# Optimization experiments

Measured on AMD Instinct MI355X. Metric: run time of the kernel, lower is better.

The kernel has to match this reference:

```python
import jax, jax.numpy as jnp
import numpy as np

B, I, H = 4096, 1024, 1024


def setup_inputs() -> dict:
    key = jax.random.key(0)
    ks = jax.random.split(key, 7)
    s = 0.1  # matches uniform(-0.1, 0.1) init scale loosely
    return {
        "input": jax.random.normal(ks[0], (B, I), jnp.float32),
        "h_t": jax.random.normal(ks[1], (B, H), jnp.float32),
        "c_t": jax.random.normal(ks[2], (B, H), jnp.float32),
        "w_i": jax.random.uniform(ks[3], (I, 4 * H), jnp.float32, -s, s),
        "w_h": jax.random.uniform(ks[4], (H, 4 * H), jnp.float32, -s, s),
        "b_i": jax.random.uniform(ks[5], (4 * H,), jnp.float32, -s, s),
        "b_h": jax.random.uniform(ks[6], (4 * H,), jnp.float32, -s, s),
    }


def reference(input, h_t, c_t, w_i, w_h, b_i, b_h):
    # ifgo: [B, 4H] = x @ w_i + h @ w_h + b_i + b_h
    ifgo = input @ w_i + h_t @ w_h + (b_i + b_h)
    i, f, g, o = jnp.split(ifgo, 4, axis=1)
    i = jax.nn.sigmoid(i)
    f = jax.nn.sigmoid(f)
    g = jnp.tanh(g)
    o = jax.nn.sigmoid(o)
    c_new = f * c_t + i * g
    h_new = o * jnp.tanh(c_new)
    return (h_new, c_new)
```

## Files before the change

### kernel.cpp

```cpp
#include <hip/hip_runtime.h>
#include <stdint.h>

typedef __attribute__((ext_vector_type(8))) short short8;
typedef __attribute__((ext_vector_type(4))) float floatx4;

__device__ inline unsigned short f2bf(float x) {
  union { float f; unsigned int u; } v; v.f = x;
  unsigned int r = v.u + 0x7FFFu + ((v.u >> 16) & 1u);
  return (unsigned short)(r >> 16);
}

__global__ void pack_a(const float* __restrict__ x, const float* __restrict__ h,
                       unsigned short* __restrict__ A) {
  int idx = blockIdx.x * 256 + threadIdx.x;
  int row = idx >> 8;
  int kc  = (idx & 255) << 3;
  const float* src = (kc < 1024) ? (x + (size_t)row * 1024 + kc)
                                 : (h + (size_t)row * 1024 + (kc - 1024));
  float4 a = ((const float4*)src)[0];
  float4 b = ((const float4*)src)[1];
  uint4 o;
  o.x = f2bf(a.x) | ((unsigned)f2bf(a.y) << 16);
  o.y = f2bf(a.z) | ((unsigned)f2bf(a.w) << 16);
  o.z = f2bf(b.x) | ((unsigned)f2bf(b.y) << 16);
  o.w = f2bf(b.z) | ((unsigned)f2bf(b.w) << 16);
  *(uint4*)(A + (size_t)row * 2048 + kc) = o;
}

__global__ void pack_w(const float* __restrict__ wi, const float* __restrict__ wh,
                       unsigned short* __restrict__ Wt) {
  __shared__ float tile[64][65];
  int kt = blockIdx.x & 31;
  int nt = blockIdx.x >> 5;
  int k0 = kt << 6, n0 = nt << 6;
  const float* src = (k0 < 1024) ? (wi + (size_t)k0 * 4096)
                                 : (wh + (size_t)(k0 - 1024) * 4096);
  int t = threadIdx.x;
  int c4 = (t & 15) << 2, rr = t >> 4;
#pragma unroll
  for (int p = 0; p < 4; ++p) {
    int kk = rr + p * 16;
    float4 v = *(const float4*)(src + (size_t)kk * 4096 + n0 + c4);
    tile[kk][c4 + 0] = v.x; tile[kk][c4 + 1] = v.y;
    tile[kk][c4 + 2] = v.z; tile[kk][c4 + 3] = v.w;
  }
  __syncthreads();
  int k8 = (t & 7) << 3, nn = t >> 3;
#pragma unroll
  for (int p = 0; p < 2; ++p) {
    int n = nn + p * 32;
    uint4 o;
    o.x = f2bf(tile[k8 + 0][n]) | ((unsigned)f2bf(tile[k8 + 1][n]) << 16);
    o.y = f2bf(tile[k8 + 2][n]) | ((unsigned)f2bf(tile[k8 + 3][n]) << 16);
    o.z = f2bf(tile[k8 + 4][n]) | ((unsigned)f2bf(tile[k8 + 5][n]) << 16);
    o.w = f2bf(tile[k8 + 6][n]) | ((unsigned)f2bf(tile[k8 + 7][n]) << 16);
    *(uint4*)(Wt + (size_t)(n0 + n) * 2048 + k0 + k8) = o;
  }
}

__device__ inline void gl_lds16(const void* g, void* l) {
  __builtin_amdgcn_global_load_lds(
      (const __attribute__((address_space(1))) void*)g,
      (__attribute__((address_space(3))) void*)l, 16, 0, 0);
}

__global__ void gemm_bt(const unsigned short* __restrict__ A,
                        const unsigned short* __restrict__ Bt,
                        float* __restrict__ C) {
  constexpr int K = 2048, N = 4096;
  __shared__ char AsB[128 * 64];
  __shared__ char BsB[128 * 64];
  const int tid  = threadIdx.x;
  const int lane = tid & 63;
  const int wave = tid >> 6;
  const int wm = wave >> 1, wn = wave & 1;
  const int m0 = blockIdx.y << 7, n0 = blockIdx.x << 7;

  const int r  = tid >> 2;
  const int cb = (tid & 3) << 4;
  const char* aS0 = (const char*)A + (size_t)(m0 + r) * K * 2 + cb;
  const char* aS1 = aS0 + (size_t)64 * K * 2;
  const char* bS0 = (const char*)Bt + (size_t)(n0 + r) * K * 2 + cb;
  const char* bS1 = bS0 + (size_t)64 * K * 2;
  char* aD0 = AsB + tid * 16;
  char* aD1 = AsB + 4096 + tid * 16;
  char* bD0 = BsB + tid * 16;
  char* bD1 = BsB + 4096 + tid * 16;

  floatx4 acc[4][4] = {};
  const int rA = (wm << 6) + (lane & 15);
  const int rB = (wn << 6) + (lane & 15);
  const int kb = (lane >> 4) << 4;

  for (int ks = 0; ks < K; ks += 32) {
    gl_lds16(aS0, aD0); gl_lds16(aS1, aD1);
    gl_lds16(bS0, bD0); gl_lds16(bS1, bD1);
    aS0 += 64; aS1 += 64; bS0 += 64; bS1 += 64;
    __syncthreads();
    short8 af[4], bfr[4];
#pragma unroll
    for (int f = 0; f < 4; ++f) {
      af[f]  = *(const short8*)(AsB + (rA + f * 16) * 64 + kb);
      bfr[f] = *(const short8*)(BsB + (rB + f * 16) * 64 + kb);
    }
#pragma unroll
    for (int i = 0; i < 4; ++i)
#pragma unroll
      for (int j = 0; j < 4; ++j)
        acc[i][j] = __builtin_amdgcn_mfma_f32_16x16x32_bf16(af[i], bfr[j], acc[i][j], 0, 0, 0);
    __syncthreads();
  }

  const int er = (lane >> 4) << 2;
  const int ec = lane & 15;
#pragma unroll
  for (int i = 0; i < 4; ++i) {
#pragma unroll
    for (int rg = 0; rg < 4; ++rg) {
      int row = m0 + (wm << 6) + i * 16 + er + rg;
      float* cp = C + (size_t)row * N + n0 + (wn << 6) + ec;
#pragma unroll
      for (int j = 0; j < 4; ++j) cp[j * 16] = acc[i][j][rg];
    }
  }
}

__device__ inline float sigm(float x)  { return 1.0f / (1.0f + __expf(-x)); }
__device__ inline float tanhx(float x) { return 2.0f / (1.0f + __expf(-2.0f * x)) - 1.0f; }

__global__ void lstm_ew(const float* __restrict__ ifgo, const float* __restrict__ ct,
                        const float* __restrict__ bi, const float* __restrict__ bh,
                        float* __restrict__ out) {
  int idx = blockIdx.x * 256 + threadIdx.x;
  int b  = idx >> 8;
  int hc = (idx & 255) << 2;
  const float* base = ifgo + (size_t)b * 4096;
  float4 zi = *(const float4*)(base + hc);
  float4 zf = *(const float4*)(base + 1024 + hc);
  float4 zg = *(const float4*)(base + 2048 + hc);
  float4 zo = *(const float4*)(base + 3072 + hc);
  float4 cv = *(const float4*)(ct + (size_t)b * 1024 + hc);
  float4 bi0 = *(const float4*)(bi + hc);
  float4 bi1 = *(const float4*)(bi + 1024 + hc);
  float4 bi2 = *(const float4*)(bi + 2048 + hc);
  float4 bi3 = *(const float4*)(bi + 3072 + hc);
  float4 bh0 = *(const float4*)(bh + hc);
  float4 bh1 = *(const float4*)(bh + 1024 + hc);
  float4 bh2 = *(const float4*)(bh + 2048 + hc);
  float4 bh3 = *(const float4*)(bh + 3072 + hc);

  const float* zia = (const float*)&zi; const float* zfa = (const float*)&zf;
  const float* zga = (const float*)&zg; const float* zoa = (const float*)&zo;
  const float* cva = (const float*)&cv;
  const float* b0a = (const float*)&bi0; const float* b1a = (const float*)&bi1;
  const float* b2a = (const float*)&bi2; const float* b3a = (const float*)&bi3;
  const float* h0a = (const float*)&bh0; const float* h1a = (const float*)&bh1;
  const float* h2a = (const float*)&bh2; const float* h3a = (const float*)&bh3;

  float4 hn, cn;
  float* hna = (float*)&hn; float* cna = (float*)&cn;
#pragma unroll
  for (int j = 0; j < 4; ++j) {
    float iv = sigm(zia[j] + b0a[j] + h0a[j]);
    float fv = sigm(zfa[j] + b1a[j] + h1a[j]);
    float gv = tanhx(zga[j] + b2a[j] + h2a[j]);
    float ov = sigm(zoa[j] + b3a[j] + h3a[j]);
    float c = fv * cva[j] + iv * gv;
    cna[j] = c;
    hna[j] = ov * tanhx(c);
  }
  size_t o = (size_t)b * 1024 + hc;
  *(float4*)(out + o) = hn;
  *(float4*)(out + 4194304 + o) = cn;
}

extern "C" void kernel_launch(void* const* d_in, const int* in_sizes, int n_in,
                              void* d_out, int out_size, void* d_ws, size_t ws_size,
                              hipStream_t stream) {
  const float* x  = (const float*)d_in[0];
  const float* ht = (const float*)d_in[1];
  const float* ct = (const float*)d_in[2];
  const float* wi = (const float*)d_in[3];
  const float* wh = (const float*)d_in[4];
  const float* bi = (const float*)d_in[5];
  const float* bh = (const float*)d_in[6];
  float* out = (float*)d_out;

  char* ws = (char*)d_ws;
  unsigned short* Abf = (unsigned short*)ws;
  unsigned short* Wbf = (unsigned short*)(ws + (16u << 20));
  float* ifgo        = (float*)(ws + (32u << 20));

  pack_a<<<4096, 256, 0, stream>>>(x, ht, Abf);
  pack_w<<<2048, 256, 0, stream>>>(wi, wh, Wbf);
  gemm_bt<<<dim3(32, 32), 256, 0, stream>>>(Abf, Wbf, ifgo);
  lstm_ew<<<4096, 256, 0, stream>>>(ifgo, ct, bi, bh, out);
}
```

Measured before the change: 234.2 us.

## Fuse LSTM gate epilogue into GEMM via gate-interleaved weight tile mapping

The GEMM now tiles the N dimension so each block loads 32 hidden units from each of the four gate slices, which puts the i/f/g/o accumulators for one hidden unit in the same thread. The bias add, activations and cell/hidden update run in the GEMM epilogue. This removes the separate elementwise kernel and the 64MB fp32 ifgo round-trip through global memory. Epilogue stores are now scalar, 16 lanes wide per row, rather than float4, and each output block does extra ct reads and transcendental math.

```diff
diff --git a/kernel.cpp b/kernel.cpp
--- a/kernel.cpp
+++ b/kernel.cpp
@@ -64,24 +64,33 @@
       (__attribute__((address_space(3))) void*)l, 16, 0, 0);
 }
 
-__global__ void gemm_bt(const unsigned short* __restrict__ A,
-                        const unsigned short* __restrict__ Bt,
-                        float* __restrict__ C) {
-  constexpr int K = 2048, N = 4096;
+__device__ inline float sigm(float x)  { return 1.0f / (1.0f + __expf(-x)); }
+__device__ inline float tanhx(float x) { return 2.0f / (1.0f + __expf(-2.0f * x)) - 1.0f; }
+
+__global__ void gemm_lstm(const unsigned short* __restrict__ A,
+                          const unsigned short* __restrict__ Bt,
+                          const float* __restrict__ ct,
+                          const float* __restrict__ bi,
+                          const float* __restrict__ bh,
+                          float* __restrict__ out) {
+  constexpr int K = 2048;
   __shared__ char AsB[128 * 64];
   __shared__ char BsB[128 * 64];
   const int tid  = threadIdx.x;
   const int lane = tid & 63;
   const int wave = tid >> 6;
   const int wm = wave >> 1, wn = wave & 1;
-  const int m0 = blockIdx.y << 7, n0 = blockIdx.x << 7;
+  const int m0 = blockIdx.y << 7;
+  const int h0 = blockIdx.x << 5;
 
   const int r  = tid >> 2;
   const int cb = (tid & 3) << 4;
   const char* aS0 = (const char*)A + (size_t)(m0 + r) * K * 2 + cb;
   const char* aS1 = aS0 + (size_t)64 * K * 2;
-  const char* bS0 = (const char*)Bt + (size_t)(n0 + r) * K * 2 + cb;
-  const char* bS1 = bS0 + (size_t)64 * K * 2;
+  const int nB0 = ((r >> 4) & 3) * 1024 + h0 + (r & 15);
+  const int nB1 = ((r >> 4) & 3) * 1024 + h0 + 16 + (r & 15);
+  const char* bS0 = (const char*)Bt + (size_t)nB0 * K * 2 + cb;
+  const char* bS1 = (const char*)Bt + (size_t)nB1 * K * 2 + cb;
   char* aD0 = AsB + tid * 16;
   char* aD1 = AsB + 4096 + tid * 16;
   char* bD0 = BsB + tid * 16;
@@ -113,65 +122,27 @@
 
   const int er = (lane >> 4) << 2;
   const int ec = lane & 15;
+  const int h  = h0 + (wn << 4) + ec;
+  float bias[4];
+#pragma unroll
+  for (int j = 0; j < 4; ++j) bias[j] = bi[j * 1024 + h] + bh[j * 1024 + h];
+
 #pragma unroll
   for (int i = 0; i < 4; ++i) {
 #pragma unroll
     for (int rg = 0; rg < 4; ++rg) {
       int row = m0 + (wm << 6) + i * 16 + er + rg;
-      float* cp = C + (size_t)row * N + n0 + (wn << 6) + ec;
-#pragma unroll
-      for (int j = 0; j < 4; ++j) cp[j * 16] = acc[i][j][rg];
+      size_t o = (size_t)row * 1024 + h;
+      float cv = ct[o];
+      float iv = sigm(acc[i][0][rg] + bias[0]);
+      float fv = sigm(acc[i][1][rg] + bias[1]);
+      float gv = tanhx(acc[i][2][rg] + bias[2]);
+      float ov = sigm(acc[i][3][rg] + bias[3]);
+      float cn = fv * cv + iv * gv;
+      out[o] = ov * tanhx(cn);
+      out[4194304 + o] = cn;
     }
   }
-}
-
-__device__ inline float sigm(float x)  { return 1.0f / (1.0f + __expf(-x)); }
-__device__ inline float tanhx(float x) { return 2.0f / (1.0f + __expf(-2.0f * x)) - 1.0f; }
-
-__global__ void lstm_ew(const float* __restrict__ ifgo, const float* __restrict__ ct,
-                        const float* __restrict__ bi, const float* __restrict__ bh,
-                        float* __restrict__ out) {
-  int idx = blockIdx.x * 256 + threadIdx.x;
-  int b  = idx >> 8;
-  int hc = (idx & 255) << 2;
-  const float* base = ifgo + (size_t)b * 4096;
-  float4 zi = *(const float4*)(base + hc);
-  float4 zf = *(const float4*)(base + 1024 + hc);
-  float4 zg = *(const float4*)(base + 2048 + hc);
-  float4 zo = *(const float4*)(base + 3072 + hc);
-  float4 cv = *(const float4*)(ct + (size_t)b * 1024 + hc);
-  float4 bi0 = *(const float4*)(bi + hc);
-  float4 bi1 = *(const float4*)(bi + 1024 + hc);
-  float4 bi2 = *(const float4*)(bi + 2048 + hc);
-  float4 bi3 = *(const float4*)(bi + 3072 + hc);
-  float4 bh0 = *(const float4*)(bh + hc);
-  float4 bh1 = *(const float4*)(bh + 1024 + hc);
-  float4 bh2 = *(const float4*)(bh + 2048 + hc);
-  float4 bh3 = *(const float4*)(bh + 3072 + hc);
-
-  const float* zia = (const float*)&zi; const float* zfa = (const float*)&zf;
-  const float* zga = (const float*)&zg; const float* zoa = (const float*)&zo;
-  const float* cva = (const float*)&cv;
-  const float* b0a = (const float*)&bi0; const float* b1a = (const float*)&bi1;
-  const float* b2a = (const float*)&bi2; const float* b3a = (const float*)&bi3;
-  const float* h0a = (const float*)&bh0; const float* h1a = (const float*)&bh1;
-  const float* h2a = (const float*)&bh2; const float* h3a = (const float*)&bh3;
-
-  float4 hn, cn;
-  float* hna = (float*)&hn; float* cna = (float*)&cn;
-#pragma unroll
-  for (int j = 0; j < 4; ++j) {
-    float iv = sigm(zia[j] + b0a[j] + h0a[j]);
-    float fv = sigm(zfa[j] + b1a[j] + h1a[j]);
-    float gv = tanhx(zga[j] + b2a[j] + h2a[j]);
-    float ov = sigm(zoa[j] + b3a[j] + h3a[j]);
-    float c = fv * cva[j] + iv * gv;
-    cna[j] = c;
-    hna[j] = ov * tanhx(c);
-  }
-  size_t o = (size_t)b * 1024 + hc;
-  *(float4*)(out + o) = hn;
-  *(float4*)(out + 4194304 + o) = cn;
 }
 
 extern "C" void kernel_launch(void* const* d_in, const int* in_sizes, int n_in,
@@ -189,10 +160,8 @@
   char* ws = (char*)d_ws;
   unsigned short* Abf = (unsigned short*)ws;
   unsigned short* Wbf = (unsigned short*)(ws + (16u << 20));
-  float* ifgo        = (float*)(ws + (32u << 20));
 
   pack_a<<<4096, 256, 0, stream>>>(x, ht, Abf);
   pack_w<<<2048, 256, 0, stream>>>(wi, wh, Wbf);
-  gemm_bt<<<dim3(32, 32), 256, 0, stream>>>(Abf, Wbf, ifgo);
-  lstm_ew<<<4096, 256, 0, stream>>>(ifgo, ct, bi, bh, out);
+  gemm_lstm<<<dim3(32, 32), 256, 0, stream>>>(Abf, Wbf, ct, bi, bh, out);
 }
```

Result: faster. 228.0 us (-2.6%).
